# Kernel optimization log

Hardware: AMD Instinct MI355X
Metric: run time of the kernel (lower is better)

## Reference

```python
import jax, jax.numpy as jnp
import numpy as np

B, T, C = 16, 512, 1024   # batch, frames, activation_dim
D = 4096                  # dict_size
K = 128                   # top-k per window
WIN = 8                   # window_size


def setup_inputs() -> dict:
    key = jax.random.key(0)
    k1, k2, k3, k4 = jax.random.split(key, 4)
    # decoder weight (C, D), columns normalized as in __init__
    W_dec = jax.random.normal(k1, (C, D), jnp.float32)
    W_dec = W_dec / jnp.linalg.norm(W_dec, axis=0, keepdims=True)
    # encoder initialized as decoder transpose (then independently perturbed to mimic training)
    W_enc = W_dec.T + 0.01 * jax.random.normal(k2, (D, C), jnp.float32)
    b_enc = 0.01 * jax.random.normal(k3, (D,), jnp.float32)
    b_dec = 0.01 * jax.random.normal(k4, (C,), jnp.float32)
    x = jax.random.normal(jax.random.fold_in(key, 7), (B, T, C), jnp.float32)
    return {"x": x, "W_enc": W_enc, "b_enc": b_enc, "W_dec": W_dec, "b_dec": b_dec}


def _window_topk(pre, k, win):
    # pre: (B, T, D) post-relu activations
    b, t, d = pre.shape
    pad = (-t) % win  # static
    if pad:
        pre_p = jnp.pad(pre, ((0, 0), (0, pad), (0, 0)))
    else:
        pre_p = pre
    tp = t + pad
    nw = tp // win
    xw = pre_p.reshape(b, nw, win, d)
    ws = xw.sum(axis=2)                        # (B, nw, D) window sums
    _, idx = jax.lax.top_k(ws, k)              # (B, nw, K)
    # scatter 1.0 at top-k dictionary entries per (batch, window) row
    idx_flat = idx.reshape(b * nw, k)
    rows = jnp.arange(b * nw)[:, None]
    mask = jnp.zeros((b * nw, d), pre.dtype).at[rows, idx_flat].set(1.0)
    mask = mask.reshape(b, nw, 1, d)
    sparse = (xw * mask).reshape(b, tp, d)[:, :t]
    return sparse


def reference(x, W_enc, b_enc, W_dec, b_dec):
    # encode: relu((x - b_dec) @ W_enc^T + b_enc)
    pre = jax.nn.relu(jnp.einsum('btc,dc->btd', x - b_dec, W_enc) + b_enc)  # (B,T,D)
    encoded = _window_topk(pre, K, WIN)                                     # (B,T,D)
    # decode: encoded @ W_dec^T + b_dec
    recon = jnp.einsum('btd,cd->btc', encoded, W_dec) + b_dec               # (B,T,C)
    return recon, encoded
```

## Files before the change

kernel.cpp:

```cpp
#include <hip/hip_runtime.h>

#define B_   16
#define T_   512
#define C_   1024
#define D_   4096
#define K_   128
#define WIN_ 8
#define NW_  (T_ / WIN_)
#define M_   (B_ * T_)

typedef __attribute__((ext_vector_type(8))) short bf16x8_t;
typedef __attribute__((ext_vector_type(4))) float f32x4_t;

__device__ __forceinline__ void gload16(const void* g, void* l) {
    __builtin_amdgcn_global_load_lds(
        (const __attribute__((address_space(1))) void*)g,
        (__attribute__((address_space(3))) void*)l, 16, 0, 0);
}

__device__ __forceinline__ unsigned short f2bf(float f) {
    unsigned u = __float_as_uint(f);
    unsigned r = (u + 0x7fffu + ((u >> 16) & 1u)) >> 16;
    return (unsigned short)r;
}
__device__ __forceinline__ float bf2f(unsigned short h) {
    return __uint_as_float((unsigned)h << 16);
}

__device__ __forceinline__ unsigned f2key(float f) {
    unsigned u = __float_as_uint(f);
    return (u & 0x80000000u) ? ~u : (u | 0x80000000u);
}
__device__ __forceinline__ float key2f(unsigned k) {
    unsigned u = (k & 0x80000000u) ? (k & 0x7fffffffu) : ~k;
    return __uint_as_float(u);
}

__global__ __launch_bounds__(256) void prep_cvt_wenc(
    const float* __restrict__ W_enc, const float* __restrict__ b_enc,
    const float* __restrict__ b_dec, unsigned short* __restrict__ wencbf,
    float* __restrict__ benc2)
{
    int d = blockIdx.x;
    int tid = threadIdx.x;
    float4 wv = ((const float4*)(W_enc + (size_t)d * C_))[tid];
    uint2 o;
    o.x = (unsigned)f2bf(wv.x) | ((unsigned)f2bf(wv.y) << 16);
    o.y = (unsigned)f2bf(wv.z) | ((unsigned)f2bf(wv.w) << 16);
    ((uint2*)(wencbf + (size_t)d * C_))[tid] = o;
    float4 bv = ((const float4*)b_dec)[tid];
    float s = wv.x * bv.x + wv.y * bv.y + wv.z * bv.z + wv.w * bv.w;
    __shared__ float red[256];
    red[tid] = s;
    __syncthreads();
    for (int off = 128; off > 0; off >>= 1) {
        if (tid < off) red[tid] += red[tid + off];
        __syncthreads();
    }
    if (tid == 0) benc2[d] = b_enc[d] - red[0];
}

__global__ void cvt_bf16(const float* __restrict__ in, unsigned short* __restrict__ out, int n8)
{
    int i = blockIdx.x * blockDim.x + threadIdx.x;
    if (i >= n8) return;
    const float4* p = (const float4*)(in + (size_t)i * 8);
    float4 a = p[0], b = p[1];
    uint4 o;
    o.x = (unsigned)f2bf(a.x) | ((unsigned)f2bf(a.y) << 16);
    o.y = (unsigned)f2bf(a.z) | ((unsigned)f2bf(a.w) << 16);
    o.z = (unsigned)f2bf(b.x) | ((unsigned)f2bf(b.y) << 16);
    o.w = (unsigned)f2bf(b.z) | ((unsigned)f2bf(b.w) << 16);
    ((uint4*)out)[i] = o;
}

__global__ void transpose_wdec(const float* __restrict__ W, unsigned short* __restrict__ WT)
{
    __shared__ float tile[32][33];
    int d0 = blockIdx.x * 32;
    int c0 = blockIdx.y * 32;
    int tx = threadIdx.x, ty = threadIdx.y;
    #pragma unroll
    for (int i = 0; i < 32; i += 8)
        tile[ty + i][tx] = W[(size_t)(c0 + ty + i) * D_ + d0 + tx];
    __syncthreads();
    #pragma unroll
    for (int i = 0; i < 32; i += 8)
        WT[(size_t)(d0 + ty + i) * C_ + c0 + tx] = f2bf(tile[tx][ty + i]);
}

__global__ __launch_bounds__(256) void mfma_gemm_dense(
    const unsigned short* __restrict__ Abf,
    const unsigned short* __restrict__ Bbf,
    const float* __restrict__ benc2,
    float* __restrict__ enc,
    float* __restrict__ wsums)
{
    __shared__ unsigned short lA[128 * 32];
    __shared__ unsigned short lB[128 * 32];
    __shared__ float cst[4][16][68];
    int tid = threadIdx.x;
    int lane = tid & 63;
    int wv = tid >> 6;
    int wm = wv >> 1, wn = wv & 1;

    int lid = blockIdx.y * gridDim.x + blockIdx.x;
    int sw = (lid & 7) * 256 + (lid >> 3);
    int bn = sw & 31, bm = sw >> 5;

    f32x4_t acc[4][4];
    #pragma unroll
    for (int i = 0; i < 4; i++)
        #pragma unroll
        for (int j = 0; j < 4; j++) acc[i][j] = (f32x4_t){0.f, 0.f, 0.f, 0.f};

    const unsigned short* Ab = Abf + (size_t)bm * 128 * C_;
    const unsigned short* Bb = Bbf + (size_t)bn * 128 * C_;

    int m_s[2], u_s[2];
    #pragma unroll
    for (int q = 0; q < 2; q++) {
        int p = q * 256 + tid;
        int m = p >> 2, v = p & 3;
        m_s[q] = m;
        u_s[q] = v ^ ((m >> 1) & 3);
    }

    int r = lane & 15, g = lane >> 4;
    for (int k0 = 0; k0 < C_; k0 += 32) {
        __syncthreads();
        #pragma unroll
        for (int q = 0; q < 2; q++) {
            gload16(Ab + (size_t)m_s[q] * C_ + k0 + u_s[q] * 8,
                    &lA[(q * 256 + wv * 64) * 8]);
            gload16(Bb + (size_t)m_s[q] * C_ + k0 + u_s[q] * 8,
                    &lB[(q * 256 + wv * 64) * 8]);
        }
        __syncthreads();
        bf16x8_t af[4], bfr[4];
        #pragma unroll
        for (int mi = 0; mi < 4; mi++) {
            int m = wm * 64 + mi * 16 + r;
            int u = g ^ ((m >> 1) & 3);
            af[mi] = *(const bf16x8_t*)&lA[m * 32 + u * 8];
        }
        #pragma unroll
        for (int ni = 0; ni < 4; ni++) {
            int d = wn * 64 + ni * 16 + r;
            int u = g ^ ((d >> 1) & 3);
            bfr[ni] = *(const bf16x8_t*)&lB[d * 32 + u * 8];
        }
        #pragma unroll
        for (int mi = 0; mi < 4; mi++)
            #pragma unroll
            for (int ni = 0; ni < 4; ni++)
                acc[mi][ni] = __builtin_amdgcn_mfma_f32_16x16x32_bf16(
                    af[mi], bfr[ni], acc[mi][ni], 0, 0, 0);
    }

    int b = bm >> 2;
    int t_blk = (bm & 3) * 128;
    int dbase = bn * 128 + wn * 64;
    int mbase_w = bm * 128 + wm * 64;
    int wbase = b * NW_ + (t_blk >> 3) + wm * 8;

    float bias_r[4];
    #pragma unroll
    for (int ni = 0; ni < 4; ni++) bias_r[ni] = benc2[dbase + ni * 16 + r];

    float wsv[4][4];
    #pragma unroll
    for (int mi = 0; mi < 4; mi++) {
        #pragma unroll
        for (int ni = 0; ni < 4; ni++) {
            float s = 0.f;
            #pragma unroll
            for (int q = 0; q < 4; q++) {
                float v = acc[mi][ni][q] + bias_r[ni];
                v = v > 0.f ? v : 0.f;
                cst[wv][g * 4 + q][ni * 16 + r] = v;
                s += v;
            }
            float partner = __shfl_xor(s, 16);
            wsv[mi][ni] = s + partner;
        }
        #pragma unroll
        for (int ri = 0; ri < 4; ri++) {
            int row = ri * 4 + (lane >> 4);
            int c4 = (lane & 15) * 4;
            float4 vv = *(const float4*)&cst[wv][row][c4];
            *(float4*)(enc + (size_t)(mbase_w + mi * 16 + row) * D_ + dbase + c4) = vv;
        }
    }

    if ((g & 1) == 0) {
        #pragma unroll
        for (int mi = 0; mi < 4; mi++)
            #pragma unroll
            for (int ni = 0; ni < 4; ni++)
                cst[wv][mi * 2 + (g >> 1)][ni * 16 + r] = wsv[mi][ni];
    }
    #pragma unroll
    for (int it = 0; it < 2; it++) {
        int row = lane >> 3;
        int c4 = (lane & 7) * 4 + it * 32;
        float4 vv = *(const float4*)&cst[wv][row][c4];
        *(float4*)(wsums + (size_t)(wbase + row) * D_ + dbase + c4) = vv;
    }
}

__device__ __forceinline__ void find_bucket(
    const int* hist, int need, int shift, unsigned pref,
    unsigned* shp, int* shn, int tid)
{
    if (tid < 64) {
        int L = tid;
        int h0 = hist[L * 4], h1 = hist[L * 4 + 1];
        int h2 = hist[L * 4 + 2], h3 = hist[L * 4 + 3];
        int s3 = h3, s2 = h2 + s3, s1 = h1 + s2, s0 = h0 + s1;
        int T = s0, I = T;
        #pragma unroll
        for (int off = 1; off < 64; off <<= 1) {
            int t = __shfl_down(I, off);
            if (L + off < 64) I += t;
        }
        int H = I - T;
        int S[5] = {H + s0, H + s1, H + s2, H + s3, H};
        #pragma unroll
        for (int j = 0; j < 4; j++) {
            if (S[j] >= need && S[j + 1] < need) {
                *shp = pref | ((unsigned)(L * 4 + j) << shift);
                *shn = need - S[j + 1];
            }
        }
    }
    __syncthreads();
}

__device__ __forceinline__ void radix_select(
    const unsigned* keys, int n, int need0, int npass, unsigned maxkey,
    int* hist, unsigned* shp, int* shn, int tid)
{
    if (tid == 0) { *shp = 0u; *shn = need0; }
    __syncthreads();
    for (int pass = 0; pass < npass; ++pass) {
        int shift = 24 - pass * 8;
        unsigned pref = *shp;
        int need = *shn;
        unsigned pmask = (pass == 0) ? 0u : (0xFFFFFFFFu << (shift + 8));
        hist[tid] = 0;
        __syncthreads();
        for (int i = tid; i < n; i += 256) {
            unsigned k = keys[i];
            if (k <= maxkey && (k & pmask) == pref)
                atomicAdd(&hist[(k >> shift) & 0xFF], 1);
        }
        __syncthreads();
        find_bucket(hist, need, shift, pref, shp, shn, tid);
    }
}

__device__ __forceinline__ int block_prefix_excl(int v, int* wsum, int tid)
{
    __syncthreads();
    int lane = tid & 63, wv = tid >> 6;
    int x = v;
    #pragma unroll
    for (int off = 1; off < 64; off <<= 1) {
        int t = __shfl_up(x, off);
        if (lane >= off) x += t;
    }
    if (lane == 63) wsum[wv] = x;
    __syncthreads();
    int base = 0;
    #pragma unroll
    for (int w2 = 0; w2 < 3; w2++) if (w2 < wv) base += wsum[w2];
    return base + x - v;
}

#define DELTA 0.15f
#define MAXCAND 320

__global__ __launch_bounds__(256) void fixup_mask_decode(
    const float* __restrict__ wsums, const float* __restrict__ x,
    const float* __restrict__ W_enc, const float* __restrict__ benc2,
    const unsigned short* __restrict__ WdTb, const float* __restrict__ b_dec,
    float* __restrict__ enc, float* __restrict__ recon)
{
    int row = blockIdx.x;
    int b = row / NW_, w = row % NW_;
    int t0g = b * T_ + w * WIN_;
    __shared__ unsigned keys[D_];
    __shared__ float xs[WIN_][C_];
    __shared__ int hist[256];
    __shared__ int wsum[4];
    __shared__ unsigned sh_prefix;
    __shared__ int sh_need;
    __shared__ int cand[MAXCAND];
    __shared__ unsigned ckeys[MAXCAND];
    __shared__ int sh_ncand, sh_nhi;
    unsigned short* hbits = (unsigned short*)hist;
    int* whist = (int*)xs;
    float (*act)[12] = (float(*)[12])xs;
    int*      sidx      = cand;
    unsigned* bmask_lds = (unsigned*)(cand + 128);
    int*      pprefix   = (int*)ckeys;
    int tid = threadIdx.x;

    for (int i = tid; i < D_ / 4; i += 256) {
        float4 v = ((const float4*)(wsums + (size_t)row * D_))[i];
        keys[i * 4 + 0] = f2key(v.x);
        keys[i * 4 + 1] = f2key(v.y);
        keys[i * 4 + 2] = f2key(v.z);
        keys[i * 4 + 3] = f2key(v.w);
    }
    for (int i = tid; i < 1024; i += 256) whist[i] = 0;
    if (tid == 0) { sh_ncand = 0; sh_nhi = 0; }
    __syncthreads();

    {
        int* myh = whist + (tid >> 6) * 256;
        for (int i = tid; i < D_; i += 256)
            atomicAdd(&myh[keys[i] >> 24], 1);
        __syncthreads();
        hist[tid] = whist[tid] + whist[256 + tid] + whist[512 + tid] + whist[768 + tid];
        __syncthreads();
        find_bucket(hist, K_, 24, 0u, &sh_prefix, &sh_need, tid);
    }
    for (int pass = 1; pass < 3; ++pass) {
        int shift = 24 - pass * 8;
        unsigned pref = sh_prefix;
        int need = sh_need;
        unsigned pmask = 0xFFFFFFFFu << (shift + 8);
        hist[tid] = 0;
        __syncthreads();
        for (int i = tid; i < D_; i += 256) {
            unsigned k = keys[i];
            if ((k & pmask) == pref)
                atomicAdd(&hist[(k >> shift) & 0xFF], 1);
        }
        __syncthreads();
        find_bucket(hist, need, shift, pref, &sh_prefix, &sh_need, tid);
    }
    float kthf = key2f(sh_prefix);
    unsigned TH_HI = f2key(kthf + DELTA);
    unsigned TH_LO = f2key(kthf - DELTA);

    for (int i = tid; i < WIN_ * C_ / 4; i += 256)
        ((float4*)xs)[i] = ((const float4*)(x + (size_t)t0g * C_))[i];
    {
        int myhi = 0;
        for (int i = tid; i < D_; i += 256) {
            unsigned k = keys[i];
            if (k > TH_HI) myhi++;
            else if (k >= TH_LO) {
                int pos = atomicAdd(&sh_ncand, 1);
                if (pos < MAXCAND) cand[pos] = i;
            }
        }
        if (myhi) atomicAdd(&sh_nhi, myhi);
    }
    __syncthreads();
    int nc = sh_ncand < MAXCAND ? sh_ncand : MAXCAND;

    {
        int wvi = tid >> 6, ln = tid & 63;
        int c0 = ln * 4;
        for (int cb = wvi; cb < nc; cb += 4) {
            int d = cand[cb];
            const float* wrow = W_enc + (size_t)d * C_;
            float a[WIN_] = {0.f, 0.f, 0.f, 0.f, 0.f, 0.f, 0.f, 0.f};
            #pragma unroll
            for (int q = 0; q < 4; q++) {
                float4 wq = *(const float4*)(wrow + q * 256 + c0);
                #pragma unroll
                for (int j = 0; j < WIN_; j++) {
                    float4 xq = *(const float4*)(&xs[j][q * 256 + c0]);
                    a[j] = fmaf(wq.x, xq.x, a[j]);
                    a[j] = fmaf(wq.y, xq.y, a[j]);
                    a[j] = fmaf(wq.z, xq.z, a[j]);
                    a[j] = fmaf(wq.w, xq.w, a[j]);
                }
            }
            #pragma unroll
            for (int off = 1; off < 64; off <<= 1)
                #pragma unroll
                for (int j = 0; j < WIN_; j++) a[j] += __shfl_xor(a[j], off);
            if (ln == 0) {
                float bias = benc2[d], s = 0.f;
                #pragma unroll
                for (int j = 0; j < WIN_; j++) {
                    float v = a[j] + bias;
                    s += v > 0.f ? v : 0.f;
                }
                unsigned k1 = f2key(s);
                keys[d] = k1;
                ckeys[cb] = k1;
            }
        }
    }
    __syncthreads();

    for (int i = tid; i < nc; i += 256)
        if (ckeys[i] > TH_HI) atomicAdd(&sh_nhi, 1);
    __syncthreads();
    int need0 = K_ - sh_nhi;
    if (need0 > 0)
        radix_select(ckeys, nc, need0, 4, TH_HI, hist, &sh_prefix, &sh_need, tid);
    else
        radix_select(keys, D_, K_, 4, 0xFFFFFFFFu, hist, &sh_prefix, &sh_need, tid);
    unsigned kth = sh_prefix;
    int need_eq = sh_need;

    int base16 = tid * 16;
    unsigned mybits = 0;
    int eqcnt = 0;
    #pragma unroll
    for (int j = 0; j < 16; ++j) {
        unsigned k = keys[base16 + j];
        if (k > kth) mybits |= (1u << j);
        else if (k == kth) eqcnt++;
    }
    int rr = block_prefix_excl(eqcnt, wsum, tid);
    #pragma unroll
    for (int j = 0; j < 16; ++j) {
        unsigned k = keys[base16 + j];
        if (k == kth) { if (rr < need_eq) mybits |= (1u << j); rr++; }
    }
    hbits[tid] = (unsigned short)mybits;
    __syncthreads();
    if (tid < 128)
        bmask_lds[tid] = (unsigned)hbits[2 * tid] | ((unsigned)hbits[2 * tid + 1] << 16);
    int pv = (tid < 128) ? __popc((unsigned)hbits[2 * tid] | ((unsigned)hbits[2 * tid + 1] << 16)) : 0;
    int ppref = block_prefix_excl(pv, wsum, tid);
    if (tid < 128) pprefix[tid] = ppref;
    int pos = block_prefix_excl(__popc(mybits), wsum, tid);
    #pragma unroll
    for (int j = 0; j < 16; ++j) {
        if (mybits & (1u << j)) sidx[pos++] = base16 + j;
    }
    __syncthreads();

    for (int jrow = 0; jrow < WIN_; jrow++) {
        float* rowp = enc + (size_t)(t0g + jrow) * D_;
        #pragma unroll
        for (int k4 = 0; k4 < 4; k4++) {
            int d4 = tid + k4 * 256;
            int widx = d4 >> 3;
            int bit0 = (d4 & 7) * 4;
            unsigned word = bmask_lds[widx];
            unsigned nib = (word >> bit0) & 0xFu;
            float4 v = {0.f, 0.f, 0.f, 0.f};
            if (nib) {
                v = ((const float4*)rowp)[d4];
                int rk = pprefix[widx] + __popc(word & ((1u << bit0) - 1u));
                float vals[4] = {v.x, v.y, v.z, v.w};
                #pragma unroll
                for (int l = 0; l < 4; l++) {
                    if (nib & (1u << l)) { act[rk][jrow] = vals[l]; rk++; }
                    else vals[l] = 0.f;
                }
                v.x = vals[0]; v.y = vals[1]; v.z = vals[2]; v.w = vals[3];
            }
            ((float4*)rowp)[d4] = v;
        }
    }
    __syncthreads();

    {
        float accv[WIN_][4] = {};
        int c0 = tid * 4;
        for (int i = 0; i < K_; i += 4) {
            int d0v = sidx[i + 0], d1v = sidx[i + 1];
            int d2v = sidx[i + 2], d3v = sidx[i + 3];
            ushort4 wu0 = *(const ushort4*)(WdTb + (size_t)d0v * C_ + c0);
            ushort4 wu1 = *(const ushort4*)(WdTb + (size_t)d1v * C_ + c0);
            ushort4 wu2 = *(const ushort4*)(WdTb + (size_t)d2v * C_ + c0);
            ushort4 wu3 = *(const ushort4*)(WdTb + (size_t)d3v * C_ + c0);
            #pragma unroll
            for (int u = 0; u < 4; u++) {
                ushort4 wu = (u == 0) ? wu0 : (u == 1) ? wu1 : (u == 2) ? wu2 : wu3;
                float4 wv = {bf2f(wu.x), bf2f(wu.y), bf2f(wu.z), bf2f(wu.w)};
                const float* ar = act[i + u];
                #pragma unroll
                for (int j = 0; j < WIN_; j++) {
                    float aj = ar[j];
                    accv[j][0] = fmaf(aj, wv.x, accv[j][0]);
                    accv[j][1] = fmaf(aj, wv.y, accv[j][1]);
                    accv[j][2] = fmaf(aj, wv.z, accv[j][2]);
                    accv[j][3] = fmaf(aj, wv.w, accv[j][3]);
                }
            }
        }
        float4 bd = *(const float4*)(b_dec + c0);
        #pragma unroll
        for (int j = 0; j < WIN_; j++) {
            float4 o;
            o.x = accv[j][0] + bd.x; o.y = accv[j][1] + bd.y;
            o.z = accv[j][2] + bd.z; o.w = accv[j][3] + bd.w;
            *(float4*)(recon + (size_t)(t0g + j) * C_ + c0) = o;
        }
    }
}

extern "C" void kernel_launch(void* const* d_in, const int* in_sizes, int n_in,
                              void* d_out, int out_size, void* d_ws, size_t ws_size,
                              hipStream_t stream)
{
    const float* x     = (const float*)d_in[0];
    const float* W_enc = (const float*)d_in[1];
    const float* b_enc = (const float*)d_in[2];
    const float* W_dec = (const float*)d_in[3];
    const float* b_dec = (const float*)d_in[4];

    float* out   = (float*)d_out;
    float* recon = out;
    float* enc   = out + (size_t)M_ * C_;

    unsigned short* xbf   = (unsigned short*)recon;
    float*          wsums = (float*)((char*)recon + (size_t)M_ * C_ * 2);

    char* ws = (char*)d_ws;
    unsigned short* WdTb    = (unsigned short*)ws;
    float*          benc2   = (float*)(ws + (size_t)D_ * C_ * 2);
    unsigned short* wencbf  = (unsigned short*)((char*)benc2 + D_ * 4);

    prep_cvt_wenc<<<D_, 256, 0, stream>>>(W_enc, b_enc, b_dec, wencbf, benc2);
    cvt_bf16<<<(M_ * C_ / 8 + 255) / 256, 256, 0, stream>>>(x, xbf, M_ * C_ / 8);
    transpose_wdec<<<dim3(D_ / 32, C_ / 32), dim3(32, 8), 0, stream>>>(W_dec, WdTb);
    mfma_gemm_dense<<<dim3(32, 64), 256, 0, stream>>>(xbf, wencbf, benc2, enc, wsums);
    fixup_mask_decode<<<B_ * NW_, 256, 0, stream>>>(
        wsums, x, W_enc, benc2, WdTb, b_dec, enc, recon);
}
```

Before: 263.6 us.

## Drop dense encoder store; recompute selected activations with MFMA in fixup kernel

The dense GEMM no longer writes the full 8192x4096 fp32 pre-activation tensor. It only emits window sums. The fixup kernel then recomputes the 128 selected features per window with a small bf16 MFMA product of W_enc rows against the window's x rows, which are already in LDS, and writes the sparse enc rows directly without reading them back. This removes about 128 MB of global write and read traffic, at the cost of extra per-block compute and a per-iteration fp32-to-bf16 conversion of x. The decode loop also batches 8 gathered W_dec loads per iteration instead of 4.

After: 247.7 us. 6.0% less time.

```diff
diff --git a/kernel.cpp b/kernel.cpp
--- a/kernel.cpp
+++ b/kernel.cpp
@@ -89,16 +89,15 @@
         WT[(size_t)(d0 + ty + i) * C_ + c0 + tx] = f2bf(tile[tx][ty + i]);
 }
 
-__global__ __launch_bounds__(256) void mfma_gemm_dense(
+__global__ __launch_bounds__(256) void mfma_gemm_ws(
     const unsigned short* __restrict__ Abf,
     const unsigned short* __restrict__ Bbf,
     const float* __restrict__ benc2,
-    float* __restrict__ enc,
     float* __restrict__ wsums)
 {
     __shared__ unsigned short lA[128 * 32];
     __shared__ unsigned short lB[128 * 32];
-    __shared__ float cst[4][16][68];
+    __shared__ float cst[4][8][68];
     int tid = threadIdx.x;
     int lane = tid & 63;
     int wv = tid >> 6;
@@ -161,14 +160,12 @@
     int b = bm >> 2;
     int t_blk = (bm & 3) * 128;
     int dbase = bn * 128 + wn * 64;
-    int mbase_w = bm * 128 + wm * 64;
     int wbase = b * NW_ + (t_blk >> 3) + wm * 8;
 
     float bias_r[4];
     #pragma unroll
     for (int ni = 0; ni < 4; ni++) bias_r[ni] = benc2[dbase + ni * 16 + r];
 
-    float wsv[4][4];
     #pragma unroll
     for (int mi = 0; mi < 4; mi++) {
         #pragma unroll
@@ -178,34 +175,20 @@
             for (int q = 0; q < 4; q++) {
                 float v = acc[mi][ni][q] + bias_r[ni];
                 v = v > 0.f ? v : 0.f;
-                cst[wv][g * 4 + q][ni * 16 + r] = v;
                 s += v;
             }
             float partner = __shfl_xor(s, 16);
-            wsv[mi][ni] = s + partner;
-        }
-        #pragma unroll
-        for (int ri = 0; ri < 4; ri++) {
-            int row = ri * 4 + (lane >> 4);
-            int c4 = (lane & 15) * 4;
-            float4 vv = *(const float4*)&cst[wv][row][c4];
-            *(float4*)(enc + (size_t)(mbase_w + mi * 16 + row) * D_ + dbase + c4) = vv;
-        }
-    }
-
-    if ((g & 1) == 0) {
-        #pragma unroll
-        for (int mi = 0; mi < 4; mi++)
-            #pragma unroll
-            for (int ni = 0; ni < 4; ni++)
-                cst[wv][mi * 2 + (g >> 1)][ni * 16 + r] = wsv[mi][ni];
+            float wsv = s + partner;
+            if ((g & 1) == 0)
+                cst[wv][mi * 2 + (g >> 1)][ni * 16 + r] = wsv;
+        }
     }
     #pragma unroll
     for (int it = 0; it < 2; it++) {
-        int row = lane >> 3;
+        int rowq = lane >> 3;
         int c4 = (lane & 7) * 4 + it * 32;
-        float4 vv = *(const float4*)&cst[wv][row][c4];
-        *(float4*)(wsums + (size_t)(wbase + row) * D_ + dbase + c4) = vv;
+        float4 vv = *(const float4*)&cst[wv][rowq][c4];
+        *(float4*)(wsums + (size_t)(wbase + rowq) * D_ + dbase + c4) = vv;
     }
 }
 
@@ -284,6 +267,7 @@
 __global__ __launch_bounds__(256) void fixup_mask_decode(
     const float* __restrict__ wsums, const float* __restrict__ x,
     const float* __restrict__ W_enc, const float* __restrict__ benc2,
+    const unsigned short* __restrict__ wencbf,
     const unsigned short* __restrict__ WdTb, const float* __restrict__ b_dec,
     float* __restrict__ enc, float* __restrict__ recon)
 {
@@ -301,7 +285,7 @@
     __shared__ int sh_ncand, sh_nhi;
     unsigned short* hbits = (unsigned short*)hist;
     int* whist = (int*)xs;
-    float (*act)[12] = (float(*)[12])xs;
+    float (*act)[12] = (float(*)[12])keys;
     int*      sidx      = cand;
     unsigned* bmask_lds = (unsigned*)(cand + 128);
     int*      pprefix   = (int*)ckeys;
@@ -441,6 +425,41 @@
     }
     __syncthreads();
 
+    {
+        int lane = tid & 63;
+        int r = lane & 15, g = lane >> 4;
+        int wvq = tid >> 6;
+        int tsrc = (r < WIN_) ? r : 0;
+        int rowA0 = sidx[(wvq * 2 + 0) * 16 + r];
+        int rowA1 = sidx[(wvq * 2 + 1) * 16 + r];
+        const unsigned short* pa0 = wencbf + (size_t)rowA0 * C_;
+        const unsigned short* pa1 = wencbf + (size_t)rowA1 * C_;
+        f32x4_t acca0 = (f32x4_t){0.f, 0.f, 0.f, 0.f};
+        f32x4_t acca1 = (f32x4_t){0.f, 0.f, 0.f, 0.f};
+        for (int k0 = 0; k0 < C_; k0 += 32) {
+            bf16x8_t bfrag;
+            #pragma unroll
+            for (int j = 0; j < 8; j++)
+                bfrag[j] = (short)f2bf(xs[tsrc][k0 + g * 8 + j]);
+            bf16x8_t a0 = *(const bf16x8_t*)(pa0 + k0 + g * 8);
+            bf16x8_t a1 = *(const bf16x8_t*)(pa1 + k0 + g * 8);
+            acca0 = __builtin_amdgcn_mfma_f32_16x16x32_bf16(a0, bfrag, acca0, 0, 0, 0);
+            acca1 = __builtin_amdgcn_mfma_f32_16x16x32_bf16(a1, bfrag, acca1, 0, 0, 0);
+        }
+        if (r < WIN_) {
+            #pragma unroll
+            for (int q = 0; q < 4; q++) {
+                int s0 = (wvq * 2 + 0) * 16 + g * 4 + q;
+                float v0 = acca0[q] + benc2[sidx[s0]];
+                act[s0][r] = v0 > 0.f ? v0 : 0.f;
+                int s1 = (wvq * 2 + 1) * 16 + g * 4 + q;
+                float v1 = acca1[q] + benc2[sidx[s1]];
+                act[s1][r] = v1 > 0.f ? v1 : 0.f;
+            }
+        }
+    }
+    __syncthreads();
+
     for (int jrow = 0; jrow < WIN_; jrow++) {
         float* rowp = enc + (size_t)(t0g + jrow) * D_;
         #pragma unroll
@@ -452,35 +471,27 @@
             unsigned nib = (word >> bit0) & 0xFu;
             float4 v = {0.f, 0.f, 0.f, 0.f};
             if (nib) {
-                v = ((const float4*)rowp)[d4];
                 int rk = pprefix[widx] + __popc(word & ((1u << bit0) - 1u));
-                float vals[4] = {v.x, v.y, v.z, v.w};
                 #pragma unroll
                 for (int l = 0; l < 4; l++) {
-                    if (nib & (1u << l)) { act[rk][jrow] = vals[l]; rk++; }
-                    else vals[l] = 0.f;
+                    if (nib & (1u << l)) { ((float*)&v)[l] = act[rk][jrow]; rk++; }
                 }
-                v.x = vals[0]; v.y = vals[1]; v.z = vals[2]; v.w = vals[3];
             }
             ((float4*)rowp)[d4] = v;
         }
     }
-    __syncthreads();
 
     {
         float accv[WIN_][4] = {};
         int c0 = tid * 4;
-        for (int i = 0; i < K_; i += 4) {
-            int d0v = sidx[i + 0], d1v = sidx[i + 1];
-            int d2v = sidx[i + 2], d3v = sidx[i + 3];
-            ushort4 wu0 = *(const ushort4*)(WdTb + (size_t)d0v * C_ + c0);
-            ushort4 wu1 = *(const ushort4*)(WdTb + (size_t)d1v * C_ + c0);
-            ushort4 wu2 = *(const ushort4*)(WdTb + (size_t)d2v * C_ + c0);
-            ushort4 wu3 = *(const ushort4*)(WdTb + (size_t)d3v * C_ + c0);
-            #pragma unroll
-            for (int u = 0; u < 4; u++) {
-                ushort4 wu = (u == 0) ? wu0 : (u == 1) ? wu1 : (u == 2) ? wu2 : wu3;
-                float4 wv = {bf2f(wu.x), bf2f(wu.y), bf2f(wu.z), bf2f(wu.w)};
+        for (int i = 0; i < K_; i += 8) {
+            ushort4 wu[8];
+            #pragma unroll
+            for (int u = 0; u < 8; u++)
+                wu[u] = *(const ushort4*)(WdTb + (size_t)sidx[i + u] * C_ + c0);
+            #pragma unroll
+            for (int u = 0; u < 8; u++) {
+                float4 wv = {bf2f(wu[u].x), bf2f(wu[u].y), bf2f(wu[u].z), bf2f(wu[u].w)};
                 const float* ar = act[i + u];
                 #pragma unroll
                 for (int j = 0; j < WIN_; j++) {
@@ -528,7 +539,7 @@
     prep_cvt_wenc<<<D_, 256, 0, stream>>>(W_enc, b_enc, b_dec, wencbf, benc2);
     cvt_bf16<<<(M_ * C_ / 8 + 255) / 256, 256, 0, stream>>>(x, xbf, M_ * C_ / 8);
     transpose_wdec<<<dim3(D_ / 32, C_ / 32), dim3(32, 8), 0, stream>>>(W_dec, WdTb);
-    mfma_gemm_dense<<<dim3(32, 64), 256, 0, stream>>>(xbf, wencbf, benc2, enc, wsums);
+    mfma_gemm_ws<<<dim3(32, 64), 256, 0, stream>>>(xbf, wencbf, benc2, wsums);
     fixup_mask_decode<<<B_ * NW_, 256, 0, stream>>>(
-        wsums, x, W_enc, benc2, WdTb, b_dec, enc, recon);
-}
+        wsums, x, W_enc, benc2, wencbf, WdTb, b_dec, enc, recon);
+}
```
